# Kernel optimization log

Measured on AMD Instinct MI355X. Metric: run time of the kernel, lower is better.

The kernel has to match this reference:

```python
import jax, jax.numpy as jnp
import numpy as np

GAMMA1 = 5.0
GAMMA2 = 5.0
ALPHA = 0.2
BETA = 1.0
K = 0.1
SEQ = 5

B = 16384
EMB = 64
ITEM_NUM = 200000
USER_NUM = 100000
CLUSTER = 64


def setup_inputs() -> dict:
    key = jax.random.key(0)
    ks = jax.random.split(key, 7)
    u = jax.random.randint(ks[0], (B,), 0, USER_NUM)
    X = jax.random.randint(ks[1], (B, SEQ), 0, ITEM_NUM + 1)
    y = jax.random.randint(ks[2], (B,), 0, ITEM_NUM + 1)
    item_emb = jax.random.normal(ks[3], (ITEM_NUM + 1, EMB), dtype=jnp.float32)
    user_emb = jax.random.normal(ks[4], (USER_NUM, EMB), dtype=jnp.float32)
    ae_raw = jax.random.normal(ks[5], (ITEM_NUM + 1, CLUSTER), dtype=jnp.float32)
    w_raw = jax.random.normal(ks[6], (CLUSTER, CLUSTER), dtype=jnp.float32)
    return {"u": u, "X": X, "y": y, "item_emb": item_emb,
            "user_emb": user_emb, "ae_raw": ae_raw, "w_raw": w_raw}


def reference(u, X, y, item_emb, user_emb, ae_raw, w_raw):
    # constructor preprocessing: _handle_ae / _filter_w
    ae = jax.nn.softmax(ae_raw * 10.0 * GAMMA1, axis=1)        # [I+1, C]
    w = jax.nn.softmax(w_raw * 100.0 * GAMMA2, axis=0)          # [C, C]
    # padding_idx=0 -> row 0 of item embedding is zero
    item_emb = item_emb.at[0].set(0.0)

    u_emb = user_emb[u]            # [B, E]
    X_emb = item_emb[X]            # [B, S, E]
    y_emb = item_emb[y]            # [B, E]

    # cluster affinity: ae[X] @ w @ ae[y]
    fac = jnp.einsum('bsc,cd,bd->bs', ae[X], w, ae[y])          # [B, S]

    # time attenuation: [0.6, 0.7, 0.8, 0.9, 1.0]
    time_factor = 1.0 - (SEQ - 1 - jnp.arange(SEQ, dtype=jnp.float32)) * K

    scores = (jnp.einsum('bse,be->bs', X_emb, y_emb)
              * BETA * jnp.exp(fac) * time_factor)              # [B, S]
    z = jax.nn.softmax(scores, axis=1)                          # [B, S]
    p = jnp.einsum('bse,bs->be', X_emb, z)                      # [B, E]
    p_u = p * ALPHA + u_emb                                     # [B, E]
    # diag(sigmoid(p_u @ y_emb.T)) == sigmoid(rowwise dot)
    return jax.nn.sigmoid(jnp.sum(p_u * y_emb, axis=-1))        # [B]
```

## Files before the change

### kernel.cpp

```cpp
#include <hip/hip_runtime.h>
#include <math.h>

#define SEQ 5
#define EMBC 64

__device__ __forceinline__ float wave_max(float v) {
    #pragma unroll
    for (int o = 32; o > 0; o >>= 1) v = fmaxf(v, __shfl_xor(v, o, 64));
    return v;
}
__device__ __forceinline__ float wave_sum(float v) {
    #pragma unroll
    for (int o = 32; o > 0; o >>= 1) v += __shfl_xor(v, o, 64);
    return v;
}

__global__ __launch_bounds__(64) void wprep_kernel(
    const float* __restrict__ w_raw, float* __restrict__ wT)
{
    const int d = blockIdx.x;
    const int c = threadIdx.x;
    float x = w_raw[c * EMBC + d] * 500.0f;
    const float m = wave_max(x);
    const float e = __expf(x - m);
    const float s = wave_sum(e);
    wT[d * EMBC + c] = e / s;
}

__global__ __launch_bounds__(256) void rumc_kernel(
    const int* __restrict__ u_idx, const int* __restrict__ X_idx,
    const int* __restrict__ y_idx,
    const float* __restrict__ item_emb, const float* __restrict__ user_emb,
    const float* __restrict__ ae_raw, const float* __restrict__ wT,
    float* __restrict__ out, int B)
{
    const int t = threadIdx.x;
    const int wave = t >> 6;
    const int lane = t & 63;
    const int b = blockIdx.x * 4 + wave;
    if (b >= B) return;

    const int yi = y_idx[b];
    const int ui = u_idx[b];
    int xi[SEQ];
    #pragma unroll
    for (int s = 0; s < SEQ; ++s) xi[s] = X_idx[b * SEQ + s];

    const float aey_r = ae_raw[yi * EMBC + lane];
    float ax_r[SEQ];
    #pragma unroll
    for (int s = 0; s < SEQ; ++s) ax_r[s] = ae_raw[xi[s] * EMBC + lane];
    const float ye_r = item_emb[yi * EMBC + lane];
    float xe[SEQ];
    #pragma unroll
    for (int s = 0; s < SEQ; ++s) xe[s] = item_emb[xi[s] * EMBC + lane];
    const float ue = user_emb[ui * EMBC + lane];

    const float ye = (yi == 0) ? 0.0f : ye_r;
    #pragma unroll
    for (int s = 0; s < SEQ; ++s) if (xi[s] == 0) xe[s] = 0.0f;

    float aey = aey_r * 50.0f;
    aey = __expf(aey - wave_max(aey));
    aey /= wave_sum(aey);

    float v = 0.0f;
    #pragma unroll
    for (int d = 0; d < EMBC; ++d)
        v = fmaf(wT[d * EMBC + lane], __shfl(aey, d, 64), v);

    float sc[SEQ];
    #pragma unroll
    for (int s = 0; s < SEQ; ++s) {
        float ax = ax_r[s] * 50.0f;
        ax = __expf(ax - wave_max(ax));
        ax /= wave_sum(ax);
        const float fac = wave_sum(ax * v);
        const float dot = wave_sum(xe[s] * ye);
        const float tf = 1.0f - (float)(SEQ - 1 - s) * 0.1f;
        sc[s] = dot * __expf(fac) * tf;
    }

    float ms = sc[0];
    #pragma unroll
    for (int s = 1; s < SEQ; ++s) ms = fmaxf(ms, sc[s]);
    float Z = 0.0f;
    #pragma unroll
    for (int s = 0; s < SEQ; ++s) { sc[s] = __expf(sc[s] - ms); Z += sc[s]; }
    const float invZ = 1.0f / Z;

    float p = 0.0f;
    #pragma unroll
    for (int s = 0; s < SEQ; ++s) p = fmaf(xe[s], sc[s] * invZ, p);
    const float pu = fmaf(p, 0.2f, ue);
    const float fin = wave_sum(pu * ye);
    if (lane == 0)
        out[b] = 1.0f / (1.0f + __expf(-fin));
}

extern "C" void kernel_launch(void* const* d_in, const int* in_sizes, int n_in,
                              void* d_out, int out_size, void* d_ws, size_t ws_size,
                              hipStream_t stream) {
    const int*   u        = (const int*)d_in[0];
    const int*   X        = (const int*)d_in[1];
    const int*   y        = (const int*)d_in[2];
    const float* item_emb = (const float*)d_in[3];
    const float* user_emb = (const float*)d_in[4];
    const float* ae_raw   = (const float*)d_in[5];
    const float* w_raw    = (const float*)d_in[6];
    float*       out      = (float*)d_out;
    float*       wT       = (float*)d_ws;

    const int B = in_sizes[0];

    wprep_kernel<<<EMBC, EMBC, 0, stream>>>(w_raw, wT);
    rumc_kernel<<<(B + 3) / 4, 256, 0, stream>>>(u, X, y, item_emb, user_emb,
                                                 ae_raw, wT, out, B);
}
```

Baseline: 165.6 us.

## Process four batch rows per wave with float4 loads and 16-lane reductions

Each wave now handles four batch elements, one per 16-lane subgroup, with each lane loading float4 vectors of embeddings and cluster affinities. Reductions shrink from 6-step 64-lane shuffles to 4-step 16-lane shuffles, and the w·ae[y] matvec runs as float4 FMAs over 16 shuffle rounds. This cuts per-row shuffle and instruction overhead and issues wider memory transactions for the gather-heavy workload. Out-of-range rows are clamped to the last valid row and their stores masked, at the cost of more registers per lane.

```diff
diff --git a/kernel.cpp b/kernel.cpp
--- a/kernel.cpp
+++ b/kernel.cpp
@@ -4,15 +4,43 @@
 #define SEQ 5
 #define EMBC 64
 
-__device__ __forceinline__ float wave_max(float v) {
+typedef float4 f4;
+
+__device__ __forceinline__ float sub_sum(float v) {
+    #pragma unroll
+    for (int o = 8; o > 0; o >>= 1) v += __shfl_xor(v, o, 64);
+    return v;
+}
+__device__ __forceinline__ float sub_max(float v) {
+    #pragma unroll
+    for (int o = 8; o > 0; o >>= 1) v = fmaxf(v, __shfl_xor(v, o, 64));
+    return v;
+}
+__device__ __forceinline__ float wave_max64(float v) {
     #pragma unroll
     for (int o = 32; o > 0; o >>= 1) v = fmaxf(v, __shfl_xor(v, o, 64));
     return v;
 }
-__device__ __forceinline__ float wave_sum(float v) {
+__device__ __forceinline__ float wave_sum64(float v) {
     #pragma unroll
     for (int o = 32; o > 0; o >>= 1) v += __shfl_xor(v, o, 64);
     return v;
+}
+__device__ __forceinline__ float dot4(f4 a, f4 b) {
+    return fmaf(a.x, b.x, fmaf(a.y, b.y, fmaf(a.z, b.z, a.w * b.w)));
+}
+__device__ __forceinline__ f4 fma4(f4 a, float s, f4 c) {
+    f4 r; r.x = fmaf(a.x, s, c.x); r.y = fmaf(a.y, s, c.y);
+          r.z = fmaf(a.z, s, c.z); r.w = fmaf(a.w, s, c.w); return r;
+}
+__device__ __forceinline__ f4 sub_softmax(f4 a, float scale) {
+    a.x *= scale; a.y *= scale; a.z *= scale; a.w *= scale;
+    const float m = sub_max(fmaxf(fmaxf(a.x, a.y), fmaxf(a.z, a.w)));
+    f4 e; e.x = __expf(a.x - m); e.y = __expf(a.y - m);
+          e.z = __expf(a.z - m); e.w = __expf(a.w - m);
+    const float inv = 1.0f / sub_sum(((e.x + e.y) + (e.z + e.w)));
+    e.x *= inv; e.y *= inv; e.z *= inv; e.w *= inv;
+    return e;
 }
 
 __global__ __launch_bounds__(64) void wprep_kernel(
@@ -21,9 +49,9 @@
     const int d = blockIdx.x;
     const int c = threadIdx.x;
     float x = w_raw[c * EMBC + d] * 500.0f;
-    const float m = wave_max(x);
+    const float m = wave_max64(x);
     const float e = __expf(x - m);
-    const float s = wave_sum(e);
+    const float s = wave_sum64(e);
     wT[d * EMBC + c] = e / s;
 }
 
@@ -34,11 +62,15 @@
     const float* __restrict__ ae_raw, const float* __restrict__ wT,
     float* __restrict__ out, int B)
 {
-    const int t = threadIdx.x;
+    const int t    = threadIdx.x;
     const int wave = t >> 6;
     const int lane = t & 63;
-    const int b = blockIdx.x * 4 + wave;
-    if (b >= B) return;
+    const int sub  = lane >> 4;
+    const int sl   = lane & 15;
+
+    int b = (blockIdx.x * 4 + wave) * 4 + sub;
+    const bool live = (b < B);
+    if (!live) b = B - 1;
 
     const int yi = y_idx[b];
     const int ui = u_idx[b];
@@ -46,37 +78,53 @@
     #pragma unroll
     for (int s = 0; s < SEQ; ++s) xi[s] = X_idx[b * SEQ + s];
 
-    const float aey_r = ae_raw[yi * EMBC + lane];
-    float ax_r[SEQ];
+    const f4* __restrict__ item4 = (const f4*)item_emb;
+    const f4* __restrict__ user4 = (const f4*)user_emb;
+    const f4* __restrict__ ae4   = (const f4*)ae_raw;
+    const f4* __restrict__ wT4   = (const f4*)wT;
+
+    f4 aey = ae4[yi * 16 + sl];
+    f4 ax[SEQ];
     #pragma unroll
-    for (int s = 0; s < SEQ; ++s) ax_r[s] = ae_raw[xi[s] * EMBC + lane];
-    const float ye_r = item_emb[yi * EMBC + lane];
-    float xe[SEQ];
+    for (int s = 0; s < SEQ; ++s) ax[s] = ae4[xi[s] * 16 + sl];
+    f4 ye = item4[yi * 16 + sl];
+    f4 xe[SEQ];
     #pragma unroll
-    for (int s = 0; s < SEQ; ++s) xe[s] = item_emb[xi[s] * EMBC + lane];
-    const float ue = user_emb[ui * EMBC + lane];
+    for (int s = 0; s < SEQ; ++s) xe[s] = item4[xi[s] * 16 + sl];
+    f4 ue = user4[ui * 16 + sl];
 
-    const float ye = (yi == 0) ? 0.0f : ye_r;
+    if (yi == 0) { ye.x = ye.y = ye.z = ye.w = 0.0f; }
     #pragma unroll
-    for (int s = 0; s < SEQ; ++s) if (xi[s] == 0) xe[s] = 0.0f;
+    for (int s = 0; s < SEQ; ++s)
+        if (xi[s] == 0) { xe[s].x = xe[s].y = xe[s].z = xe[s].w = 0.0f; }
 
-    float aey = aey_r * 50.0f;
-    aey = __expf(aey - wave_max(aey));
-    aey /= wave_sum(aey);
+    aey = sub_softmax(aey, 50.0f);
 
-    float v = 0.0f;
+    f4 v; v.x = v.y = v.z = v.w = 0.0f;
+    const int base = lane & 48;
     #pragma unroll
-    for (int d = 0; d < EMBC; ++d)
-        v = fmaf(wT[d * EMBC + lane], __shfl(aey, d, 64), v);
+    for (int dd = 0; dd < 16; ++dd) {
+        f4 ad;
+        ad.x = __shfl(aey.x, base + dd, 64);
+        ad.y = __shfl(aey.y, base + dd, 64);
+        ad.z = __shfl(aey.z, base + dd, 64);
+        ad.w = __shfl(aey.w, base + dd, 64);
+        const f4 w0 = wT4[(dd * 4 + 0) * 16 + sl];
+        const f4 w1 = wT4[(dd * 4 + 1) * 16 + sl];
+        const f4 w2 = wT4[(dd * 4 + 2) * 16 + sl];
+        const f4 w3 = wT4[(dd * 4 + 3) * 16 + sl];
+        v = fma4(w0, ad.x, v);
+        v = fma4(w1, ad.y, v);
+        v = fma4(w2, ad.z, v);
+        v = fma4(w3, ad.w, v);
+    }
 
     float sc[SEQ];
     #pragma unroll
     for (int s = 0; s < SEQ; ++s) {
-        float ax = ax_r[s] * 50.0f;
-        ax = __expf(ax - wave_max(ax));
-        ax /= wave_sum(ax);
-        const float fac = wave_sum(ax * v);
-        const float dot = wave_sum(xe[s] * ye);
+        const f4 a = sub_softmax(ax[s], 50.0f);
+        const float fac = sub_sum(dot4(a, v));
+        const float dot = sub_sum(dot4(xe[s], ye));
         const float tf = 1.0f - (float)(SEQ - 1 - s) * 0.1f;
         sc[s] = dot * __expf(fac) * tf;
     }
@@ -89,12 +137,12 @@
     for (int s = 0; s < SEQ; ++s) { sc[s] = __expf(sc[s] - ms); Z += sc[s]; }
     const float invZ = 1.0f / Z;
 
-    float p = 0.0f;
+    f4 p; p.x = p.y = p.z = p.w = 0.0f;
     #pragma unroll
-    for (int s = 0; s < SEQ; ++s) p = fmaf(xe[s], sc[s] * invZ, p);
-    const float pu = fmaf(p, 0.2f, ue);
-    const float fin = wave_sum(pu * ye);
-    if (lane == 0)
+    for (int s = 0; s < SEQ; ++s) p = fma4(xe[s], sc[s] * invZ, p);
+    const f4 pu = fma4(p, 0.2f, ue);
+    const float fin = sub_sum(dot4(pu, ye));
+    if (live && sl == 0)
         out[b] = 1.0f / (1.0f + __expf(-fin));
 }
 
@@ -114,6 +162,6 @@
     const int B = in_sizes[0];
 
     wprep_kernel<<<EMBC, EMBC, 0, stream>>>(w_raw, wT);
-    rumc_kernel<<<(B + 3) / 4, 256, 0, stream>>>(u, X, y, item_emb, user_emb,
-                                                 ae_raw, wT, out, B);
+    rumc_kernel<<<(B + 15) / 16, 256, 0, stream>>>(u, X, y, item_emb, user_emb,
+                                                   ae_raw, wT, out, B);
 }
```

Result: faster. 147.4 us (-11.0%).
